# Optimization experiments

Hardware: AMD Instinct MI355X
Metric: run time of the kernel (lower is better)

The kernel has to match this reference:

```python
import jax, jax.numpy as jnp
import numpy as np

PATCH = 5
DIM = 256
HEADS = 8
EPS = 1e-5


def split_patches(t, p):
    # t: [B,H,W,C] -> overlapping patches [B,H,W,p,p,C], stride 1, zero-pad p//2
    pad = p // 2
    tp = jnp.pad(t, ((0, 0), (pad, pad), (pad, pad), (0, 0)))
    H, W = t.shape[1], t.shape[2]
    rows = jnp.arange(H)[:, None] + jnp.arange(p)[None, :]  # [H,p]
    cols = jnp.arange(W)[:, None] + jnp.arange(p)[None, :]  # [W,p]
    return tp[:, rows[:, None, :, None], cols[None, :, None, :], :]


def layernorm(v, g, b):
    mu = jnp.mean(v, axis=-1, keepdims=True)
    var = jnp.var(v, axis=-1, keepdims=True)
    return (v - mu) * jax.lax.rsqrt(var + EPS) * g + b


def mha(q, k, v, w, b, mask):
    # w: [4,D,D] stacked (Wq,Wk,Wv,Wo), b: [4,D]; q:[N,Lq,D], k,v:[N,Lk,D]
    N, Lq, D = q.shape
    dh = D // HEADS
    qh = (q @ w[0] + b[0]).reshape(N, Lq, HEADS, dh)
    kh = (k @ w[1] + b[1]).reshape(N, -1, HEADS, dh)
    vh = (v @ w[2] + b[2]).reshape(N, -1, HEADS, dh)
    sc = jnp.einsum('nqhd,nkhd->nhqk', qh, kh) * (1.0 / float(np.sqrt(dh)))
    if mask is not None:
        sc = jnp.where(mask, sc, jnp.asarray(-1e9, sc.dtype))
    a = jax.nn.softmax(sc, axis=-1)
    o = jnp.einsum('nhqk,nkhd->nqhd', a, vh).reshape(N, Lq, D)
    return o @ w[3] + b[3], a


def setup_inputs() -> dict:
    key = jax.random.key(0)
    ks = jax.random.split(key, 10)
    B, H, W, D = 1, 64, 64, DIM
    x = jax.random.normal(ks[0], (B, H, W, D), dtype=jnp.float32)
    memory = jax.random.normal(ks[1], (B, H, W, D), dtype=jnp.float32)
    active_nodes = jax.random.randint(ks[2], (B, H, W), 0, 2).astype(bool)
    s = 0.05
    return {
        'x': x, 'memory': memory, 'active_nodes': active_nodes,
        'attn_w': jax.random.normal(ks[3], (4, D, D), dtype=jnp.float32) * s,
        'attn_b': jnp.zeros((4, D), dtype=jnp.float32),
        'pattn_w': jax.random.normal(ks[4], (4, D, D), dtype=jnp.float32) * s,
        'pattn_b': jnp.zeros((4, D), dtype=jnp.float32),
        'ff_w1': jax.random.normal(ks[5], (D, 2 * D), dtype=jnp.float32) * s,
        'ff_b1': jnp.zeros((2 * D,), dtype=jnp.float32),
        'ff_w2': jax.random.normal(ks[6], (2 * D, D), dtype=jnp.float32) * s,
        'ff_b2': jnp.zeros((D,), dtype=jnp.float32),
        'ln_g': jnp.ones((3, D), dtype=jnp.float32),   # norm1, norm2, norm3
        'ln_b': jnp.zeros((3, D), dtype=jnp.float32),
    }


def reference(x, memory, active_nodes, attn_w, attn_b, pattn_w, pattn_b,
              ff_w1, ff_b1, ff_w2, ff_b2, ln_g, ln_b):
    B, H, W, D = x.shape
    p = PATCH
    center = p // 2
    L = p * p
    cp = L // 2  # flattened center point

    act = active_nodes[..., None]                      # [B,H,W,1] bool
    ap = split_patches(act, p)                         # [B,H,W,p,p,1]
    # faithful to source: zeroes the entire patch at GRID position (center,center)
    ap = ap.at[:, center, center].set(False)
    wo_center = jnp.any(ap.reshape(B, H, W, L, 1), axis=3)  # [B,H,W,1]
    act = jnp.logical_and(wo_center, act)
    ap = split_patches(act, p)                         # recomputed with updated mask

    xp = split_patches(x, p) * ap                      # zero inactive neighbors
    xp = xp.reshape(B, H, W, L, D)
    mp = split_patches(memory, p).reshape(B, H, W, L, D)
    mask = ap[..., 0].reshape(B, H, W, L)

    N = B * H * W
    keys = xp.reshape(N, L, D)
    mem = mp.reshape(N, L, D)
    q = keys[:, cp:cp + 1, :]                          # [N,1,D]
    m = mask.reshape(N, L)[:, None, None, :]           # [N,1,1,L]

    # EncoderLayer (eval mode: dropout = identity)
    s_, attn = mha(q, keys, keys, attn_w, attn_b, m)
    s = layernorm(q + s_, ln_g[0], ln_b[0])            # norm1
    s_, _ = mha(s, mem, mem, pattn_w, pattn_b, None)
    s = layernorm(s + s_, ln_g[2], ln_b[2])            # norm3
    ff = jax.nn.relu(s @ ff_w1 + ff_b1) @ ff_w2 + ff_b2
    s = layernorm(s + ff, ln_g[1], ln_b[1])            # norm2

    out = jnp.where(act, s[:, 0, :].reshape(B, H, W, D), jnp.asarray(0.0, x.dtype))
    return out, act[..., 0]
```

## Files before the change

kernel.cpp:

```cpp
#include <hip/hip_runtime.h>
#include <math.h>

#define D 256
#define H2 512
#define HEADS 8
#define L 25
#define GH 64
#define GW 64
#define NN 4096
#define EPS 1e-5f
#define SCALE 0.17677669529663687f
#define NND 1048576

typedef __attribute__((ext_vector_type(8))) short short8;
typedef __attribute__((ext_vector_type(4))) float f32x4;

__device__ __forceinline__ bool act_at(const int* __restrict__ active, int h, int w) {
    if (h < 0 || h >= GH || w < 0 || w >= GW) return false;
    if (h == 2 && w == 2) return false;
    return active[h * GW + w] != 0;
}

__device__ __forceinline__ unsigned short f2b(float f) {
    unsigned u = __float_as_uint(f);
    u += 0x7fffu + ((u >> 16) & 1u);
    return (unsigned short)(u >> 16);
}
__device__ __forceinline__ float b2f(short v) {
    return __uint_as_float(((unsigned)(unsigned short)v) << 16);
}

__global__ __launch_bounds__(256)
void prep_kernel(const float* __restrict__ x, const float* __restrict__ mem,
                 const int* __restrict__ active,
                 const float* __restrict__ attn_w, const float* __restrict__ pattn_w,
                 const float* __restrict__ ff_w1, const float* __restrict__ ff_w2,
                 const float* __restrict__ pattn_b,
                 unsigned short* __restrict__ xmB, unsigned short* __restrict__ memB,
                 unsigned short* __restrict__ wB,
                 unsigned short* __restrict__ k2bias, unsigned short* __restrict__ v2bias) {
    const int tid = threadIdx.x;
    const int bid = blockIdx.x;
    if (bid < 192) {
        __shared__ float tile[64][65];
        const float* src; unsigned short* dst;
        int i0, n0, srcLen, dstLen;
        if (bid < 128) {
            int mat = bid >> 4, t16 = bid & 15;
            i0 = (t16 >> 2) * 64; n0 = (t16 & 3) * 64;
            src = (mat < 4) ? (attn_w + mat * 65536) : (pattn_w + (mat - 4) * 65536);
            dst = wB + mat * 65536;
            srcLen = 256; dstLen = 256;
        } else if (bid < 160) {
            int t = bid - 128;
            i0 = (t >> 3) * 64; n0 = (t & 7) * 64;
            src = ff_w1; dst = wB + 524288;
            srcLen = 512; dstLen = 256;
        } else {
            int t = bid - 160;
            i0 = (t >> 2) * 64; n0 = (t & 3) * 64;
            src = ff_w2; dst = wB + 655360;
            srcLen = 256; dstLen = 512;
        }
        int c = tid & 63, r4 = tid >> 6;
        for (int rr = 0; rr < 64; rr += 4)
            tile[rr + r4][c] = src[(size_t)(i0 + rr + r4) * srcLen + n0 + c];
        __syncthreads();
        for (int rr = 0; rr < 64; rr += 4) {
            int r = rr + r4;
            dst[(size_t)(n0 + r) * dstLen + i0 + c] = f2b(tile[c][r]);
        }
    } else {
        const int t0 = (bid - 192) * 256 + tid;
        for (int t = t0; t < 524800; t += 512 * 256) {
            if (t < 262144) {
                int n = t >> 6;
                bool a = act_at(active, n >> 6, n & 63);
                float4 v = ((const float4*)x)[t];
                ushort4 u;
                u.x = f2b(a ? v.x : 0.0f); u.y = f2b(a ? v.y : 0.0f);
                u.z = f2b(a ? v.z : 0.0f); u.w = f2b(a ? v.w : 0.0f);
                ((ushort4*)xmB)[t] = u;
            } else if (t < 524288) {
                int tt = t - 262144;
                float4 v = ((const float4*)mem)[tt];
                ushort4 u;
                u.x = f2b(v.x); u.y = f2b(v.y); u.z = f2b(v.z); u.w = f2b(v.w);
                ((ushort4*)memB)[tt] = u;
            } else {
                int tt = t - 524288;
                if (tt < 256) k2bias[tt] = f2b(pattn_b[256 + tt]);
                else          v2bias[tt - 256] = f2b(pattn_b[512 + (tt - 256)]);
            }
        }
    }
}

__global__ __launch_bounds__(256)
void proj_gemm(const unsigned short* __restrict__ xmB,
               const unsigned short* __restrict__ memB,
               const unsigned short* __restrict__ wB,
               const float* __restrict__ attn_b, const float* __restrict__ pattn_b,
               unsigned short* __restrict__ q1b, unsigned short* __restrict__ k1b,
               unsigned short* __restrict__ v1b, unsigned short* __restrict__ k2b,
               unsigned short* __restrict__ v2b) {
    const int s  = blockIdx.y >> 2;
    const int n0 = (blockIdx.y & 3) * 64;
    const unsigned short* A  = (s < 3) ? xmB : memB;
    const int wtIdx = (s < 3) ? s : (s + 2);
    const unsigned short* WT = wB + (size_t)wtIdx * 65536;
    const float* bias = (s < 3) ? (attn_b + s * 256) : (pattn_b + (s - 2) * 256);
    unsigned short* outB;
    switch (s) { case 0: outB = q1b; break; case 1: outB = k1b; break;
                 case 2: outB = v1b; break; case 3: outB = k2b; break;
                 default: outB = v2b; }

    const int tid = threadIdx.x;
    const int wave = tid >> 6, lane = tid & 63;
    const int m0 = blockIdx.x * 64 + wave * 16;
    const int lr = lane & 15;
    const int lk = (lane >> 4) << 3;
    f32x4 acc[4] = {};
    const unsigned short* arow = A  + (size_t)(m0 + lr) * 256 + lk;
    const unsigned short* brow = WT + (size_t)(n0 + lr) * 256 + lk;
    #pragma unroll
    for (int kk = 0; kk < 256; kk += 32) {
        short8 a = *(const short8*)(arow + kk);
        #pragma unroll
        for (int nf = 0; nf < 4; ++nf) {
            short8 b = *(const short8*)(brow + (size_t)nf * 16 * 256 + kk);
            acc[nf] = __builtin_amdgcn_mfma_f32_16x16x32_bf16(a, b, acc[nf], 0, 0, 0);
        }
    }
    const int rbase = m0 + ((lane >> 4) << 2);
    #pragma unroll
    for (int nf = 0; nf < 4; ++nf) {
        int c = n0 + nf * 16 + lr;
        float bc = bias[c];
        #pragma unroll
        for (int jj = 0; jj < 4; ++jj)
            outB[(size_t)(rbase + jj) * 256 + c] = f2b(acc[nf][jj] + bc);
    }
}

#define KV_OFF   0
#define ACT_OFF  51200
#define WGT_OFF  51328
#define REDA_OFF 64128
#define REDB_OFF 64640
#define STAT_OFF 65152
#define SMEM_SZ  65280
#define T1B_OFF  0
#define SB_OFF   8448
#define S2F_OFF  8448
#define S2B_OFF  25088
#define HB_OFF   33536

__device__ __forceinline__ void load_union(const unsigned short* __restrict__ base,
                                           int h, int w0, int fallback,
                                           unsigned short (*kvU)[256], int tid) {
    for (int c = tid; c < 3200; c += 512) {
        int u = c >> 5, part = c & 31;
        int r = u / 20;
        int hh = h - 2 + r, ww = w0 - 2 + (u - r * 20);
        bool ib = ((unsigned)hh < GH) && ((unsigned)ww < GW);
        int row = ib ? ((hh << 6) | ww) : fallback;
        *(uint4*)&kvU[u][part * 8] = *(const uint4*)(base + (size_t)row * 256 + part * 8);
    }
}

__global__ __launch_bounds__(512)
void head_kernel(const int* __restrict__ active, const float* __restrict__ x,
                 const unsigned short* __restrict__ wB,
                 const float* __restrict__ attn_b, const float* __restrict__ pattn_b,
                 const float* __restrict__ ln_g, const float* __restrict__ ln_b,
                 const unsigned short* __restrict__ q1b,
                 const unsigned short* __restrict__ k1b,
                 const unsigned short* __restrict__ v1b,
                 float* __restrict__ S, unsigned short* __restrict__ T2b) {
    const int tid = threadIdx.x;
    const int wv = tid >> 6, lane = tid & 63;
    const int lr = lane & 15, qi = lane >> 4;
    const int n0 = blockIdx.x * 16;
    const int h = n0 >> 6, w0 = n0 & 63;

    __shared__ __align__(16) char smem[SMEM_SZ];
    unsigned short (*kvU)[256] = (unsigned short(*)[256])(smem + KV_OFF);
    unsigned char* actU        = (unsigned char*)(smem + ACT_OFF);
    float (*wgt)[8][25]        = (float(*)[8][25])(smem + WGT_OFF);
    float (*redA)[8]           = (float(*)[8])(smem + REDA_OFF);
    float (*redB)[8]           = (float(*)[8])(smem + REDB_OFF);
    float (*stats)[2]          = (float(*)[2])(smem + STAT_OFF);
    unsigned short (*T1b)[264] = (unsigned short(*)[264])(smem + T1B_OFF);
    unsigned short (*Sb)[264]  = (unsigned short(*)[264])(smem + SB_OFF);

    if (tid < 100) {
        int r = tid / 20;
        int hh = h - 2 + r, ww = w0 - 2 + (tid - r * 20);
        actU[tid] = act_at(active, hh, ww) ? 1 : 0;
    }
    load_union(k1b, h, w0, 0, kvU, tid);
    __syncthreads();

    const int half = lane >> 5, lam = lane & 31;
    const int m = wv * 2 + half;
    float q[8];
    {
        short8 qv = *(const short8*)(q1b + (size_t)(n0 + m) * 256 + lam * 8);
        #pragma unroll
        for (int j = 0; j < 8; ++j) q[j] = b2f(qv[j]);
    }
    #pragma unroll 5
    for (int l = 0; l < L; ++l) {
        int u = (l / 5) * 20 + m + (l % 5);
        short8 kv = *(const short8*)&kvU[u][lam * 8];
        float p = q[0] * b2f(kv[0]);
        #pragma unroll
        for (int j = 1; j < 8; ++j) p = fmaf(q[j], b2f(kv[j]), p);
        p += __shfl_xor(p, 1); p += __shfl_xor(p, 2);
        float sv = actU[u] ? p * SCALE : -1e30f;
        if ((lam & 3) == 0) wgt[m][lam >> 2][l] = sv;
    }
    __syncthreads();
    if (tid < 128) {
        int mm = tid >> 3, hd = tid & 7;
        float mx = -1e30f;
        for (int l = 0; l < L; ++l) mx = fmaxf(mx, wgt[mm][hd][l]);
        float sum = 0.0f;
        for (int l = 0; l < L; ++l) { float e = expf(wgt[mm][hd][l] - mx); wgt[mm][hd][l] = e; sum += e; }
        float inv = 1.0f / sum;
        for (int l = 0; l < L; ++l) wgt[mm][hd][l] *= inv;
    }
    __syncthreads();
    load_union(v1b, h, w0, 0, kvU, tid);
    __syncthreads();
    float o[8] = {0.f,0.f,0.f,0.f,0.f,0.f,0.f,0.f};
    #pragma unroll 5
    for (int l = 0; l < L; ++l) {
        int u = (l / 5) * 20 + m + (l % 5);
        if (actU[u]) {
            float wt = wgt[m][lam >> 2][l];
            short8 v8 = *(const short8*)&kvU[u][lam * 8];
            #pragma unroll
            for (int j = 0; j < 8; ++j) o[j] = fmaf(wt, b2f(v8[j]), o[j]);
        }
    }
    __syncthreads();
    {
        unsigned short u8[8];
        #pragma unroll
        for (int j = 0; j < 8; ++j) u8[j] = f2b(o[j]);
        *(uint4*)&T1b[m][lam * 8] = *(uint4*)u8;
    }
    __syncthreads();

    {
        const unsigned short* Wo1T = wB + 3 * 65536;
        f32x4 acc[2] = {};
        #pragma unroll
        for (int kk = 0; kk < 256; kk += 32) {
            short8 a = *(const short8*)&T1b[lr][qi * 8 + kk];
            #pragma unroll
            for (int nf = 0; nf < 2; ++nf) {
                short8 b = *(const short8*)(Wo1T + (size_t)(wv * 32 + nf * 16 + lr) * 256 + qi * 8 + kk);
                acc[nf] = __builtin_amdgcn_mfma_f32_16x16x32_bf16(a, b, acc[nf], 0, 0, 0);
            }
        }
        float v[2][4], s1[4] = {0.f,0.f,0.f,0.f}, s2[4] = {0.f,0.f,0.f,0.f};
        #pragma unroll
        for (int nf = 0; nf < 2; ++nf) {
            int c = wv * 32 + nf * 16 + lr;
            float bc = attn_b[768 + c];
            #pragma unroll
            for (int jj = 0; jj < 4; ++jj) {
                int row = n0 + qi * 4 + jj;
                float vv = acc[nf][jj] + bc + x[(size_t)row * D + c];
                v[nf][jj] = vv; s1[jj] += vv; s2[jj] += vv * vv;
            }
        }
        #pragma unroll
        for (int jj = 0; jj < 4; ++jj) {
            #pragma unroll
            for (int off = 1; off < 16; off <<= 1) {
                s1[jj] += __shfl_xor(s1[jj], off);
                s2[jj] += __shfl_xor(s2[jj], off);
            }
        }
        if (lr == 0) {
            #pragma unroll
            for (int jj = 0; jj < 4; ++jj) { redA[qi*4+jj][wv] = s1[jj]; redB[qi*4+jj][wv] = s2[jj]; }
        }
        __syncthreads();
        if (tid < 16) {
            float a1 = 0.f, a2 = 0.f;
            #pragma unroll
            for (int q8 = 0; q8 < 8; ++q8) { a1 += redA[tid][q8]; a2 += redB[tid][q8]; }
            float mu = a1 * (1.0f / D);
            float var = a2 * (1.0f / D) - mu * mu;
            stats[tid][0] = mu; stats[tid][1] = rsqrtf(var + EPS);
        }
        __syncthreads();
        #pragma unroll
        for (int nf = 0; nf < 2; ++nf) {
            int c = wv * 32 + nf * 16 + lr;
            float gg = ln_g[c], bb = ln_b[c];
            #pragma unroll
            for (int jj = 0; jj < 4; ++jj) {
                int ridx = qi * 4 + jj;
                float ov = (v[nf][jj] - stats[ridx][0]) * stats[ridx][1] * gg + bb;
                S[(size_t)(n0 + ridx) * D + c] = ov;
                Sb[ridx][c] = f2b(ov);
            }
        }
    }
    __syncthreads();

    {
        const unsigned short* Wq2T = wB + 4 * 65536;
        f32x4 acc[2] = {};
        #pragma unroll
        for (int kk = 0; kk < 256; kk += 32) {
            short8 a = *(const short8*)&Sb[lr][qi * 8 + kk];
            #pragma unroll
            for (int nf = 0; nf < 2; ++nf) {
                short8 b = *(const short8*)(Wq2T + (size_t)(wv * 32 + nf * 16 + lr) * 256 + qi * 8 + kk);
                acc[nf] = __builtin_amdgcn_mfma_f32_16x16x32_bf16(a, b, acc[nf], 0, 0, 0);
            }
        }
        #pragma unroll
        for (int nf = 0; nf < 2; ++nf) {
            int c = wv * 32 + nf * 16 + lr;
            float bc = pattn_b[c];
            #pragma unroll
            for (int jj = 0; jj < 4; ++jj)
                T2b[(size_t)(n0 + qi * 4 + jj) * 256 + c] = f2b(acc[nf][jj] + bc);
        }
    }
}

__global__ __launch_bounds__(512)
void tail_kernel(const int* __restrict__ active,
                 const unsigned short* __restrict__ wB,
                 const float* __restrict__ pattn_b, const float* __restrict__ ff_b1,
                 const float* __restrict__ ff_b2,
                 const float* __restrict__ ln_g, const float* __restrict__ ln_b,
                 const unsigned short* __restrict__ k2b,
                 const unsigned short* __restrict__ v2b,
                 const float* __restrict__ S, const unsigned short* __restrict__ T2b,
                 float* __restrict__ out) {
    const int tid = threadIdx.x;
    const int wv = tid >> 6, lane = tid & 63;
    const int lr = lane & 15, qi = lane >> 4;
    const int n0 = blockIdx.x * 16;
    const int h = n0 >> 6, w0 = n0 & 63;

    __shared__ __align__(16) char smem[SMEM_SZ];
    unsigned short (*kvU)[256] = (unsigned short(*)[256])(smem + KV_OFF);
    float (*wgt)[8][25]        = (float(*)[8][25])(smem + WGT_OFF);
    float (*redA)[8]           = (float(*)[8])(smem + REDA_OFF);
    float (*redB)[8]           = (float(*)[8])(smem + REDB_OFF);
    float (*stats)[2]          = (float(*)[2])(smem + STAT_OFF);
    unsigned short (*T3b)[264] = (unsigned short(*)[264])(smem + T1B_OFF);
    float (*S2f)[260]          = (float(*)[260])(smem + S2F_OFF);
    unsigned short (*S2b)[264] = (unsigned short(*)[264])(smem + S2B_OFF);
    unsigned short (*Hb)[520]  = (unsigned short(*)[520])(smem + HB_OFF);

    load_union(k2b, h, w0, NN, kvU, tid);
    __syncthreads();

    const int half = lane >> 5, lam = lane & 31;
    const int m = wv * 2 + half;
    float q[8];
    {
        short8 qv = *(const short8*)(T2b + (size_t)(n0 + m) * 256 + lam * 8);
        #pragma unroll
        for (int j = 0; j < 8; ++j) q[j] = b2f(qv[j]);
    }
    #pragma unroll 5
    for (int l = 0; l < L; ++l) {
        int u = (l / 5) * 20 + m + (l % 5);
        short8 kv = *(const short8*)&kvU[u][lam * 8];
        float p = q[0] * b2f(kv[0]);
        #pragma unroll
        for (int j = 1; j < 8; ++j) p = fmaf(q[j], b2f(kv[j]), p);
        p += __shfl_xor(p, 1); p += __shfl_xor(p, 2);
        if ((lam & 3) == 0) wgt[m][lam >> 2][l] = p * SCALE;
    }
    __syncthreads();
    if (tid < 128) {
        int mm = tid >> 3, hd = tid & 7;
        float mx = -1e30f;
        for (int l = 0; l < L; ++l) mx = fmaxf(mx, wgt[mm][hd][l]);
        float sum = 0.0f;
        for (int l = 0; l < L; ++l) { float e = expf(wgt[mm][hd][l] - mx); wgt[mm][hd][l] = e; sum += e; }
        float inv = 1.0f / sum;
        for (int l = 0; l < L; ++l) wgt[mm][hd][l] *= inv;
    }
    __syncthreads();
    load_union(v2b, h, w0, NN, kvU, tid);
    __syncthreads();
    float o[8] = {0.f,0.f,0.f,0.f,0.f,0.f,0.f,0.f};
    #pragma unroll 5
    for (int l = 0; l < L; ++l) {
        int u = (l / 5) * 20 + m + (l % 5);
        float wt = wgt[m][lam >> 2][l];
        short8 v8 = *(const short8*)&kvU[u][lam * 8];
        #pragma unroll
        for (int j = 0; j < 8; ++j) o[j] = fmaf(wt, b2f(v8[j]), o[j]);
    }
    __syncthreads();
    {
        unsigned short u8[8];
        #pragma unroll
        for (int j = 0; j < 8; ++j) u8[j] = f2b(o[j]);
        *(uint4*)&T3b[m][lam * 8] = *(uint4*)u8;
    }
    __syncthreads();

    {
        const unsigned short* Wo2T = wB + 7 * 65536;
        f32x4 acc[2] = {};
        #pragma unroll
        for (int kk = 0; kk < 256; kk += 32) {
            short8 a = *(const short8*)&T3b[lr][qi * 8 + kk];
            #pragma unroll
            for (int nf = 0; nf < 2; ++nf) {
                short8 b = *(const short8*)(Wo2T + (size_t)(wv * 32 + nf * 16 + lr) * 256 + qi * 8 + kk);
                acc[nf] = __builtin_amdgcn_mfma_f32_16x16x32_bf16(a, b, acc[nf], 0, 0, 0);
            }
        }
        float v[2][4], s1[4] = {0.f,0.f,0.f,0.f}, s2[4] = {0.f,0.f,0.f,0.f};
        #pragma unroll
        for (int nf = 0; nf < 2; ++nf) {
            int c = wv * 32 + nf * 16 + lr;
            float bc = pattn_b[768 + c];
            #pragma unroll
            for (int jj = 0; jj < 4; ++jj) {
                int row = n0 + qi * 4 + jj;
                float vv = acc[nf][jj] + bc + S[(size_t)row * D + c];
                v[nf][jj] = vv; s1[jj] += vv; s2[jj] += vv * vv;
            }
        }
        #pragma unroll
        for (int jj = 0; jj < 4; ++jj) {
            #pragma unroll
            for (int off = 1; off < 16; off <<= 1) {
                s1[jj] += __shfl_xor(s1[jj], off);
                s2[jj] += __shfl_xor(s2[jj], off);
            }
        }
        if (lr == 0) {
            #pragma unroll
            for (int jj = 0; jj < 4; ++jj) { redA[qi*4+jj][wv] = s1[jj]; redB[qi*4+jj][wv] = s2[jj]; }
        }
        __syncthreads();
        if (tid < 16) {
            float a1 = 0.f, a2 = 0.f;
            #pragma unroll
            for (int q8 = 0; q8 < 8; ++q8) { a1 += redA[tid][q8]; a2 += redB[tid][q8]; }
            float mu = a1 * (1.0f / D);
            float var = a2 * (1.0f / D) - mu * mu;
            stats[tid][0] = mu; stats[tid][1] = rsqrtf(var + EPS);
        }
        __syncthreads();
        #pragma unroll
        for (int nf = 0; nf < 2; ++nf) {
            int c = wv * 32 + nf * 16 + lr;
            float gg = ln_g[512 + c], bb = ln_b[512 + c];
            #pragma unroll
            for (int jj = 0; jj < 4; ++jj) {
                int ridx = qi * 4 + jj;
                float ov = (v[nf][jj] - stats[ridx][0]) * stats[ridx][1] * gg + bb;
                S2f[ridx][c] = ov;
                S2b[ridx][c] = f2b(ov);
            }
        }
    }
    __syncthreads();

    {
        const unsigned short* W1T = wB + 524288;
        f32x4 acc[4] = {};
        #pragma unroll
        for (int kk = 0; kk < 256; kk += 32) {
            short8 a = *(const short8*)&S2b[lr][qi * 8 + kk];
            #pragma unroll
            for (int nf = 0; nf < 4; ++nf) {
                short8 b = *(const short8*)(W1T + (size_t)(wv * 64 + nf * 16 + lr) * 256 + qi * 8 + kk);
                acc[nf] = __builtin_amdgcn_mfma_f32_16x16x32_bf16(a, b, acc[nf], 0, 0, 0);
            }
        }
        #pragma unroll
        for (int nf = 0; nf < 4; ++nf) {
            int c = wv * 64 + nf * 16 + lr;
            float bc = ff_b1[c];
            #pragma unroll
            for (int jj = 0; jj < 4; ++jj)
                Hb[qi * 4 + jj][c] = f2b(fmaxf(acc[nf][jj] + bc, 0.0f));
        }
    }
    __syncthreads();

    {
        const unsigned short* W2T = wB + 655360;
        f32x4 acc[2] = {};
        #pragma unroll
        for (int kk = 0; kk < 512; kk += 32) {
            short8 a = *(const short8*)&Hb[lr][qi * 8 + kk];
            #pragma unroll
            for (int nf = 0; nf < 2; ++nf) {
                short8 b = *(const short8*)(W2T + (size_t)(wv * 32 + nf * 16 + lr) * 512 + qi * 8 + kk);
                acc[nf] = __builtin_amdgcn_mfma_f32_16x16x32_bf16(a, b, acc[nf], 0, 0, 0);
            }
        }
        float v[2][4], s1[4] = {0.f,0.f,0.f,0.f}, s2[4] = {0.f,0.f,0.f,0.f};
        #pragma unroll
        for (int nf = 0; nf < 2; ++nf) {
            int c = wv * 32 + nf * 16 + lr;
            float bc = ff_b2[c];
            #pragma unroll
            for (int jj = 0; jj < 4; ++jj) {
                int ridx = qi * 4 + jj;
                float vv = acc[nf][jj] + bc + S2f[ridx][c];
                v[nf][jj] = vv; s1[jj] += vv; s2[jj] += vv * vv;
            }
        }
        #pragma unroll
        for (int jj = 0; jj < 4; ++jj) {
            #pragma unroll
            for (int off = 1; off < 16; off <<= 1) {
                s1[jj] += __shfl_xor(s1[jj], off);
                s2[jj] += __shfl_xor(s2[jj], off);
            }
        }
        if (lr == 0) {
            #pragma unroll
            for (int jj = 0; jj < 4; ++jj) { redA[qi*4+jj][wv] = s1[jj]; redB[qi*4+jj][wv] = s2[jj]; }
        }
        __syncthreads();
        if (tid < 16) {
            float a1 = 0.f, a2 = 0.f;
            #pragma unroll
            for (int q8 = 0; q8 < 8; ++q8) { a1 += redA[tid][q8]; a2 += redB[tid][q8]; }
            float mu = a1 * (1.0f / D);
            float var = a2 * (1.0f / D) - mu * mu;
            stats[tid][0] = mu; stats[tid][1] = rsqrtf(var + EPS);
        }
        __syncthreads();
        bool arow_act[4];
        #pragma unroll
        for (int jj = 0; jj < 4; ++jj) {
            int row = n0 + qi * 4 + jj;
            arow_act[jj] = act_at(active, row >> 6, row & 63);
        }
        #pragma unroll
        for (int nf = 0; nf < 2; ++nf) {
            int c = wv * 32 + nf * 16 + lr;
            float gg = ln_g[256 + c], bb = ln_b[256 + c];
            #pragma unroll
            for (int jj = 0; jj < 4; ++jj) {
                int ridx = qi * 4 + jj;
                float ov = (v[nf][jj] - stats[ridx][0]) * stats[ridx][1] * gg + bb;
                out[(size_t)(n0 + ridx) * D + c] = arow_act[jj] ? ov : 0.0f;
            }
        }
        if (tid < 16) {
            int row = n0 + tid;
            out[(size_t)NND + row] = act_at(active, row >> 6, row & 63) ? 1.0f : 0.0f;
        }
    }
}

extern "C" void kernel_launch(void* const* d_in, const int* in_sizes, int n_in,
                              void* d_out, int out_size, void* d_ws, size_t ws_size,
                              hipStream_t stream) {
    const float* x       = (const float*)d_in[0];
    const float* memory  = (const float*)d_in[1];
    const int*   active  = (const int*)d_in[2];
    const float* attn_w  = (const float*)d_in[3];
    const float* attn_b  = (const float*)d_in[4];
    const float* pattn_w = (const float*)d_in[5];
    const float* pattn_b = (const float*)d_in[6];
    const float* ff_w1   = (const float*)d_in[7];
    const float* ff_b1   = (const float*)d_in[8];
    const float* ff_w2   = (const float*)d_in[9];
    const float* ff_b2   = (const float*)d_in[10];
    const float* ln_g    = (const float*)d_in[11];
    const float* ln_b    = (const float*)d_in[12];
    float* out = (float*)d_out;

    unsigned short* wsb = (unsigned short*)d_ws;
    unsigned short* xmB  = wsb;
    unsigned short* memB = wsb + (size_t)NND;
    unsigned short* wB   = wsb + 2 * (size_t)NND;
    unsigned short* q1b  = wB + 786432;
    unsigned short* k1b  = q1b + (size_t)NND;
    unsigned short* v1b  = k1b + (size_t)NND;
    unsigned short* k2b  = v1b + (size_t)NND;
    unsigned short* v2b  = k2b + (size_t)NND + 256;
    unsigned short* T2b  = v2b + (size_t)NND + 256;
    float* S = (float*)(T2b + (size_t)NND);

    hipLaunchKernelGGL(prep_kernel, dim3(704), dim3(256), 0, stream,
                       x, memory, active, attn_w, pattn_w, ff_w1, ff_w2, pattn_b,
                       xmB, memB, wB, k2b + (size_t)NND, v2b + (size_t)NND);
    hipLaunchKernelGGL(proj_gemm, dim3(64, 20), dim3(256), 0, stream,
                       xmB, memB, wB, attn_b, pattn_b, q1b, k1b, v1b, k2b, v2b);
    hipLaunchKernelGGL(head_kernel, dim3(256), dim3(512), 0, stream,
                       active, x, wB, attn_b, pattn_b, ln_g, ln_b,
                       q1b, k1b, v1b, S, T2b);
    hipLaunchKernelGGL(tail_kernel, dim3(256), dim3(512), 0, stream,
                       active, wB, pattn_b, ff_b1, ff_b2, ln_g, ln_b,
                       k2b, v2b, S, T2b, out);
}
```

Measured before the change: 93.24 us.

## Fuse head and tail kernels into one kernel keeping intermediates on-chip

Merges the head and tail kernels into a single fused kernel. The residual S and the second-attention query T2 now stay in registers and shared memory instead of round-tripping through global memory, which also removes one kernel launch. Block indices are remapped with a swizzle across the 256 blocks. The cost is higher register pressure from carrying sreg/s2reg across stages and a few extra barriers.

```diff
diff --git a/kernel.cpp b/kernel.cpp
--- a/kernel.cpp
+++ b/kernel.cpp
@@ -152,9 +152,7 @@
 #define SMEM_SZ  65280
 #define T1B_OFF  0
 #define SB_OFF   8448
-#define S2F_OFF  8448
-#define S2B_OFF  25088
-#define HB_OFF   33536
+#define HB_OFF   16896
 
 __device__ __forceinline__ void load_union(const unsigned short* __restrict__ base,
                                            int h, int w0, int fallback,
@@ -170,19 +168,25 @@
 }
 
 __global__ __launch_bounds__(512)
-void head_kernel(const int* __restrict__ active, const float* __restrict__ x,
-                 const unsigned short* __restrict__ wB,
-                 const float* __restrict__ attn_b, const float* __restrict__ pattn_b,
-                 const float* __restrict__ ln_g, const float* __restrict__ ln_b,
-                 const unsigned short* __restrict__ q1b,
-                 const unsigned short* __restrict__ k1b,
-                 const unsigned short* __restrict__ v1b,
-                 float* __restrict__ S, unsigned short* __restrict__ T2b) {
+void fused_kernel(const int* __restrict__ active, const float* __restrict__ x,
+                  const unsigned short* __restrict__ wB,
+                  const float* __restrict__ attn_b, const float* __restrict__ pattn_b,
+                  const float* __restrict__ ff_b1, const float* __restrict__ ff_b2,
+                  const float* __restrict__ ln_g, const float* __restrict__ ln_b,
+                  const unsigned short* __restrict__ q1b,
+                  const unsigned short* __restrict__ k1b,
+                  const unsigned short* __restrict__ v1b,
+                  const unsigned short* __restrict__ k2b,
+                  const unsigned short* __restrict__ v2b,
+                  float* __restrict__ out) {
     const int tid = threadIdx.x;
     const int wv = tid >> 6, lane = tid & 63;
     const int lr = lane & 15, qi = lane >> 4;
-    const int n0 = blockIdx.x * 16;
+    const int bid = ((blockIdx.x & 7) << 5) | (blockIdx.x >> 3);
+    const int n0 = bid * 16;
     const int h = n0 >> 6, w0 = n0 & 63;
+    const int half = lane >> 5, lam = lane & 31;
+    const int m = wv * 2 + half;
 
     __shared__ __align__(16) char smem[SMEM_SZ];
     unsigned short (*kvU)[256] = (unsigned short(*)[256])(smem + KV_OFF);
@@ -193,6 +197,7 @@
     float (*stats)[2]          = (float(*)[2])(smem + STAT_OFF);
     unsigned short (*T1b)[264] = (unsigned short(*)[264])(smem + T1B_OFF);
     unsigned short (*Sb)[264]  = (unsigned short(*)[264])(smem + SB_OFF);
+    unsigned short (*Hb)[520]  = (unsigned short(*)[520])(smem + HB_OFF);
 
     if (tid < 100) {
         int r = tid / 20;
@@ -202,24 +207,22 @@
     load_union(k1b, h, w0, 0, kvU, tid);
     __syncthreads();
 
-    const int half = lane >> 5, lam = lane & 31;
-    const int m = wv * 2 + half;
-    float q[8];
-    {
+    {
+        float q[8];
         short8 qv = *(const short8*)(q1b + (size_t)(n0 + m) * 256 + lam * 8);
         #pragma unroll
         for (int j = 0; j < 8; ++j) q[j] = b2f(qv[j]);
-    }
-    #pragma unroll 5
-    for (int l = 0; l < L; ++l) {
-        int u = (l / 5) * 20 + m + (l % 5);
-        short8 kv = *(const short8*)&kvU[u][lam * 8];
-        float p = q[0] * b2f(kv[0]);
-        #pragma unroll
-        for (int j = 1; j < 8; ++j) p = fmaf(q[j], b2f(kv[j]), p);
-        p += __shfl_xor(p, 1); p += __shfl_xor(p, 2);
-        float sv = actU[u] ? p * SCALE : -1e30f;
-        if ((lam & 3) == 0) wgt[m][lam >> 2][l] = sv;
+        #pragma unroll 5
+        for (int l = 0; l < L; ++l) {
+            int u = (l / 5) * 20 + m + (l % 5);
+            short8 kv = *(const short8*)&kvU[u][lam * 8];
+            float p = q[0] * b2f(kv[0]);
+            #pragma unroll
+            for (int j = 1; j < 8; ++j) p = fmaf(q[j], b2f(kv[j]), p);
+            p += __shfl_xor(p, 1); p += __shfl_xor(p, 2);
+            float sv = actU[u] ? p * SCALE : -1e30f;
+            if ((lam & 3) == 0) wgt[m][lam >> 2][l] = sv;
+        }
     }
     __syncthreads();
     if (tid < 128) {
@@ -234,19 +237,19 @@
     __syncthreads();
     load_union(v1b, h, w0, 0, kvU, tid);
     __syncthreads();
-    float o[8] = {0.f,0.f,0.f,0.f,0.f,0.f,0.f,0.f};
-    #pragma unroll 5
-    for (int l = 0; l < L; ++l) {
-        int u = (l / 5) * 20 + m + (l % 5);
-        if (actU[u]) {
-            float wt = wgt[m][lam >> 2][l];
-            short8 v8 = *(const short8*)&kvU[u][lam * 8];
-            #pragma unroll
-            for (int j = 0; j < 8; ++j) o[j] = fmaf(wt, b2f(v8[j]), o[j]);
-        }
-    }
-    __syncthreads();
-    {
+    {
+        float o[8] = {0.f,0.f,0.f,0.f,0.f,0.f,0.f,0.f};
+        #pragma unroll 5
+        for (int l = 0; l < L; ++l) {
+            int u = (l / 5) * 20 + m + (l % 5);
+            if (actU[u]) {
+                float wt = wgt[m][lam >> 2][l];
+                short8 v8 = *(const short8*)&kvU[u][lam * 8];
+                #pragma unroll
+                for (int j = 0; j < 8; ++j) o[j] = fmaf(wt, b2f(v8[j]), o[j]);
+            }
+        }
+        __syncthreads();
         unsigned short u8[8];
         #pragma unroll
         for (int j = 0; j < 8; ++j) u8[j] = f2b(o[j]);
@@ -254,6 +257,7 @@
     }
     __syncthreads();
 
+    float sreg[2][4];
     {
         const unsigned short* Wo1T = wB + 3 * 65536;
         f32x4 acc[2] = {};
@@ -308,7 +312,7 @@
             for (int jj = 0; jj < 4; ++jj) {
                 int ridx = qi * 4 + jj;
                 float ov = (v[nf][jj] - stats[ridx][0]) * stats[ridx][1] * gg + bb;
-                S[(size_t)(n0 + ridx) * D + c] = ov;
+                sreg[nf][jj] = ov;
                 Sb[ridx][c] = f2b(ov);
             }
         }
@@ -327,62 +331,35 @@
                 acc[nf] = __builtin_amdgcn_mfma_f32_16x16x32_bf16(a, b, acc[nf], 0, 0, 0);
             }
         }
+        __syncthreads();
         #pragma unroll
         for (int nf = 0; nf < 2; ++nf) {
             int c = wv * 32 + nf * 16 + lr;
             float bc = pattn_b[c];
             #pragma unroll
             for (int jj = 0; jj < 4; ++jj)
-                T2b[(size_t)(n0 + qi * 4 + jj) * 256 + c] = f2b(acc[nf][jj] + bc);
-        }
-    }
-}
-
-__global__ __launch_bounds__(512)
-void tail_kernel(const int* __restrict__ active,
-                 const unsigned short* __restrict__ wB,
-                 const float* __restrict__ pattn_b, const float* __restrict__ ff_b1,
-                 const float* __restrict__ ff_b2,
-                 const float* __restrict__ ln_g, const float* __restrict__ ln_b,
-                 const unsigned short* __restrict__ k2b,
-                 const unsigned short* __restrict__ v2b,
-                 const float* __restrict__ S, const unsigned short* __restrict__ T2b,
-                 float* __restrict__ out) {
-    const int tid = threadIdx.x;
-    const int wv = tid >> 6, lane = tid & 63;
-    const int lr = lane & 15, qi = lane >> 4;
-    const int n0 = blockIdx.x * 16;
-    const int h = n0 >> 6, w0 = n0 & 63;
-
-    __shared__ __align__(16) char smem[SMEM_SZ];
-    unsigned short (*kvU)[256] = (unsigned short(*)[256])(smem + KV_OFF);
-    float (*wgt)[8][25]        = (float(*)[8][25])(smem + WGT_OFF);
-    float (*redA)[8]           = (float(*)[8])(smem + REDA_OFF);
-    float (*redB)[8]           = (float(*)[8])(smem + REDB_OFF);
-    float (*stats)[2]          = (float(*)[2])(smem + STAT_OFF);
-    unsigned short (*T3b)[264] = (unsigned short(*)[264])(smem + T1B_OFF);
-    float (*S2f)[260]          = (float(*)[260])(smem + S2F_OFF);
-    unsigned short (*S2b)[264] = (unsigned short(*)[264])(smem + S2B_OFF);
-    unsigned short (*Hb)[520]  = (unsigned short(*)[520])(smem + HB_OFF);
-
+                T1b[qi * 4 + jj][c] = f2b(acc[nf][jj] + bc);
+        }
+    }
+    __syncthreads();
+
+    float q2[8];
+    {
+        short8 qv = *(const short8*)&T1b[m][lam * 8];
+        #pragma unroll
+        for (int j = 0; j < 8; ++j) q2[j] = b2f(qv[j]);
+    }
+    __syncthreads();
     load_union(k2b, h, w0, NN, kvU, tid);
     __syncthreads();
 
-    const int half = lane >> 5, lam = lane & 31;
-    const int m = wv * 2 + half;
-    float q[8];
-    {
-        short8 qv = *(const short8*)(T2b + (size_t)(n0 + m) * 256 + lam * 8);
-        #pragma unroll
-        for (int j = 0; j < 8; ++j) q[j] = b2f(qv[j]);
-    }
     #pragma unroll 5
     for (int l = 0; l < L; ++l) {
         int u = (l / 5) * 20 + m + (l % 5);
         short8 kv = *(const short8*)&kvU[u][lam * 8];
-        float p = q[0] * b2f(kv[0]);
-        #pragma unroll
-        for (int j = 1; j < 8; ++j) p = fmaf(q[j], b2f(kv[j]), p);
+        float p = q2[0] * b2f(kv[0]);
+        #pragma unroll
+        for (int j = 1; j < 8; ++j) p = fmaf(q2[j], b2f(kv[j]), p);
         p += __shfl_xor(p, 1); p += __shfl_xor(p, 2);
         if ((lam & 3) == 0) wgt[m][lam >> 2][l] = p * SCALE;
     }
@@ -399,30 +376,31 @@
     __syncthreads();
     load_union(v2b, h, w0, NN, kvU, tid);
     __syncthreads();
-    float o[8] = {0.f,0.f,0.f,0.f,0.f,0.f,0.f,0.f};
-    #pragma unroll 5
-    for (int l = 0; l < L; ++l) {
-        int u = (l / 5) * 20 + m + (l % 5);
-        float wt = wgt[m][lam >> 2][l];
-        short8 v8 = *(const short8*)&kvU[u][lam * 8];
-        #pragma unroll
-        for (int j = 0; j < 8; ++j) o[j] = fmaf(wt, b2f(v8[j]), o[j]);
-    }
-    __syncthreads();
-    {
+    {
+        float o[8] = {0.f,0.f,0.f,0.f,0.f,0.f,0.f,0.f};
+        #pragma unroll 5
+        for (int l = 0; l < L; ++l) {
+            int u = (l / 5) * 20 + m + (l % 5);
+            float wt = wgt[m][lam >> 2][l];
+            short8 v8 = *(const short8*)&kvU[u][lam * 8];
+            #pragma unroll
+            for (int j = 0; j < 8; ++j) o[j] = fmaf(wt, b2f(v8[j]), o[j]);
+        }
+        __syncthreads();
         unsigned short u8[8];
         #pragma unroll
         for (int j = 0; j < 8; ++j) u8[j] = f2b(o[j]);
-        *(uint4*)&T3b[m][lam * 8] = *(uint4*)u8;
-    }
-    __syncthreads();
-
+        *(uint4*)&T1b[m][lam * 8] = *(uint4*)u8;
+    }
+    __syncthreads();
+
+    float s2reg[2][4];
     {
         const unsigned short* Wo2T = wB + 7 * 65536;
         f32x4 acc[2] = {};
         #pragma unroll
         for (int kk = 0; kk < 256; kk += 32) {
-            short8 a = *(const short8*)&T3b[lr][qi * 8 + kk];
+            short8 a = *(const short8*)&T1b[lr][qi * 8 + kk];
             #pragma unroll
             for (int nf = 0; nf < 2; ++nf) {
                 short8 b = *(const short8*)(Wo2T + (size_t)(wv * 32 + nf * 16 + lr) * 256 + qi * 8 + kk);
@@ -436,8 +414,7 @@
             float bc = pattn_b[768 + c];
             #pragma unroll
             for (int jj = 0; jj < 4; ++jj) {
-                int row = n0 + qi * 4 + jj;
-                float vv = acc[nf][jj] + bc + S[(size_t)row * D + c];
+                float vv = acc[nf][jj] + bc + sreg[nf][jj];
                 v[nf][jj] = vv; s1[jj] += vv; s2[jj] += vv * vv;
             }
         }
@@ -471,8 +448,8 @@
             for (int jj = 0; jj < 4; ++jj) {
                 int ridx = qi * 4 + jj;
                 float ov = (v[nf][jj] - stats[ridx][0]) * stats[ridx][1] * gg + bb;
-                S2f[ridx][c] = ov;
-                S2b[ridx][c] = f2b(ov);
+                s2reg[nf][jj] = ov;
+                Sb[ridx][c] = f2b(ov);
             }
         }
     }
@@ -483,7 +460,7 @@
         f32x4 acc[4] = {};
         #pragma unroll
         for (int kk = 0; kk < 256; kk += 32) {
-            short8 a = *(const short8*)&S2b[lr][qi * 8 + kk];
+            short8 a = *(const short8*)&Sb[lr][qi * 8 + kk];
             #pragma unroll
             for (int nf = 0; nf < 4; ++nf) {
                 short8 b = *(const short8*)(W1T + (size_t)(wv * 64 + nf * 16 + lr) * 256 + qi * 8 + kk);
@@ -520,8 +497,7 @@
             float bc = ff_b2[c];
             #pragma unroll
             for (int jj = 0; jj < 4; ++jj) {
-                int ridx = qi * 4 + jj;
-                float vv = acc[nf][jj] + bc + S2f[ridx][c];
+                float vv = acc[nf][jj] + bc + s2reg[nf][jj];
                 v[nf][jj] = vv; s1[jj] += vv; s2[jj] += vv * vv;
             }
         }
@@ -598,18 +574,13 @@
     unsigned short* v1b  = k1b + (size_t)NND;
     unsigned short* k2b  = v1b + (size_t)NND;
     unsigned short* v2b  = k2b + (size_t)NND + 256;
-    unsigned short* T2b  = v2b + (size_t)NND + 256;
-    float* S = (float*)(T2b + (size_t)NND);
 
     hipLaunchKernelGGL(prep_kernel, dim3(704), dim3(256), 0, stream,
                        x, memory, active, attn_w, pattn_w, ff_w1, ff_w2, pattn_b,
                        xmB, memB, wB, k2b + (size_t)NND, v2b + (size_t)NND);
     hipLaunchKernelGGL(proj_gemm, dim3(64, 20), dim3(256), 0, stream,
                        xmB, memB, wB, attn_b, pattn_b, q1b, k1b, v1b, k2b, v2b);
-    hipLaunchKernelGGL(head_kernel, dim3(256), dim3(512), 0, stream,
-                       active, x, wB, attn_b, pattn_b, ln_g, ln_b,
-                       q1b, k1b, v1b, S, T2b);
-    hipLaunchKernelGGL(tail_kernel, dim3(256), dim3(512), 0, stream,
-                       active, wB, pattn_b, ff_b1, ff_b2, ln_g, ln_b,
-                       k2b, v2b, S, T2b, out);
-}
+    hipLaunchKernelGGL(fused_kernel, dim3(256), dim3(512), 0, stream,
+                       active, x, wB, attn_b, pattn_b, ff_b1, ff_b2, ln_g, ln_b,
+                       q1b, k1b, v1b, k2b, v2b, out);
+}
```

Result: faster. 91.11 us (-2.3%).
